# Optimization experiments

Hardware: AMD Instinct MI355X
Metric: run time of the kernel (lower is better)

Reference implementation:

```python
import jax, jax.numpy as jnp
import numpy as np

B, Q, K, A, H, C, O = 32, 512, 512, 256, 8, 32, 256  # batch, queries, keys, channels, heads, head_dim, out_dim


def setup_inputs() -> dict:
    key = jax.random.key(0)
    ks = jax.random.split(key, 12)
    s = 0.02
    return {
        "q_data": jax.random.normal(ks[0], (B, Q, A), jnp.float32),
        "m_data": jax.random.normal(ks[1], (B, K, A), jnp.float32),
        "bias": jax.random.normal(ks[2], (B, 1, 1, K), jnp.float32),
        "nonbatched_bias": jax.random.normal(ks[3], (H, Q, K), jnp.float32),
        "batched_bias": jax.random.normal(ks[4], (B, H, Q, K), jnp.float32),
        "query_w": jax.random.normal(ks[5], (A, H, C), jnp.float32) * s,
        "key_w": jax.random.normal(ks[6], (A, H, C), jnp.float32) * s,
        "value_w": jax.random.normal(ks[7], (A, H, C), jnp.float32) * s,
        "gating_w": jax.random.normal(ks[8], (A, H, C), jnp.float32) * s,
        "gating_b": jnp.ones((H, C), jnp.float32),
        "output_w": jax.random.normal(ks[9], (H, C, O), jnp.float32) * s,
        "output_b": jnp.zeros((O,), jnp.float32),
    }


def reference(q_data, m_data, bias, nonbatched_bias, batched_bias,
              query_w, key_w, value_w, gating_w, gating_b, output_w, output_b):
    key_scale = query_w.shape[-1] ** -0.5
    q = jnp.einsum('bqa,ahc->bqhc', q_data, query_w) * key_scale
    k = jnp.einsum('bka,ahc->bkhc', m_data, key_w)
    v = jnp.einsum('bka,ahc->bkhc', m_data, value_w)
    logits = jnp.einsum('bqhc,bkhc->bhqk', q, k) + bias
    logits = logits + nonbatched_bias[None] + batched_bias
    weights = jax.nn.softmax(logits, axis=-1)
    weighted_avg = jnp.einsum('bhqk,bkhc->bqhc', weights, v)
    gate = jax.nn.sigmoid(jnp.einsum('bqc,chv->bqhv', q_data, gating_w) + gating_b)
    weighted_avg = weighted_avg * gate
    return jnp.einsum('bqhc,hco->bqo', weighted_avg, output_w) + output_b
```

## Files before the change

### kernel.cpp

```cpp
#include <hip/hip_runtime.h>
#include <cstdint>
#include <cstddef>


typedef __attribute__((ext_vector_type(8))) short short8;
typedef __attribute__((ext_vector_type(4))) float f32x4;
typedef __attribute__((ext_vector_type(4))) unsigned int u32x4;
typedef __attribute__((ext_vector_type(2))) unsigned int u32x2;

#define DEVFN static __device__ __forceinline__
#define L2E 1.4426950408889634f

DEVFN unsigned short f2b(float f) {
  unsigned int u = __builtin_bit_cast(unsigned int, f);
  u += 0x7fffu + ((u >> 16) & 1u);
  return (unsigned short)(u >> 16);
}
DEVFN float b2f(unsigned int bits16) {
  return __builtin_bit_cast(float, bits16 << 16);
}
DEVFN unsigned int pack2(float a, float b) {
  return (unsigned int)f2b(a) | ((unsigned int)f2b(b) << 16);
}
DEVFN f32x4 mfma16(short8 a, short8 b, f32x4 c) {
  return __builtin_amdgcn_mfma_f32_16x16x32_bf16(a, b, c, 0, 0, 0);
}

__global__ __launch_bounds__(256) void wtrans_kernel(
    const float* __restrict__ qw, const float* __restrict__ kw,
    const float* __restrict__ vw, const float* __restrict__ gw,
    const float* __restrict__ ow,
    unsigned short* __restrict__ wtq, unsigned short* __restrict__ wtk,
    unsigned short* __restrict__ wtv, unsigned short* __restrict__ wtg,
    unsigned short* __restrict__ wt3)
{
  const int matid = blockIdx.x >> 4;
  const int tile  = blockIdx.x & 15;
  const float* src = (matid == 0) ? qw : (matid == 1) ? kw : (matid == 2) ? vw
                   : (matid == 3) ? gw : ow;
  unsigned short* dst = (matid == 0) ? wtq : (matid == 1) ? wtk : (matid == 2) ? wtv
                      : (matid == 3) ? wtg : wt3;
  const int tr = (tile >> 2) * 64, tc = (tile & 3) * 64;
  __shared__ unsigned short T[64 * 72];
  const int t = threadIdx.x;
  {
    const int row = t >> 2, cb = (t & 3) * 16;
#pragma unroll
    for (int ii = 0; ii < 4; ++ii) {
      f32x4 v = *(const f32x4*)&src[(size_t)(tr + row) * 256 + tc + cb + ii * 4];
      u32x2 p; p.x = pack2(v.x, v.y); p.y = pack2(v.z, v.w);
      *(u32x2*)&T[row * 72 + cb + ii * 4] = p;
    }
  }
  __syncthreads();
  {
    const int c0 = t >> 2, rb = (t & 3) * 16;
    unsigned short vals[16];
#pragma unroll
    for (int m = 0; m < 16; ++m) vals[m] = T[(rb + m) * 72 + c0];
    u32x4 s0, s1;
    s0.x = (unsigned)vals[0]  | ((unsigned)vals[1]  << 16);
    s0.y = (unsigned)vals[2]  | ((unsigned)vals[3]  << 16);
    s0.z = (unsigned)vals[4]  | ((unsigned)vals[5]  << 16);
    s0.w = (unsigned)vals[6]  | ((unsigned)vals[7]  << 16);
    s1.x = (unsigned)vals[8]  | ((unsigned)vals[9]  << 16);
    s1.y = (unsigned)vals[10] | ((unsigned)vals[11] << 16);
    s1.z = (unsigned)vals[12] | ((unsigned)vals[13] << 16);
    s1.w = (unsigned)vals[14] | ((unsigned)vals[15] << 16);
    unsigned short* dp = &dst[(size_t)(tc + c0) * 256 + tr + rb];
    *(u32x4*)dp = s0;
    *(u32x4*)(dp + 8) = s1;
  }
}

__global__ __launch_bounds__(512, 4) void proj_kernel(
    const float* __restrict__ q_data, const float* __restrict__ m_data,
    const unsigned short* __restrict__ wtq, const unsigned short* __restrict__ wtk,
    const unsigned short* __restrict__ wtv, const unsigned short* __restrict__ wtg,
    const float* __restrict__ gating_b,
    unsigned short* __restrict__ qp, unsigned short* __restrict__ kp,
    unsigned short* __restrict__ vp, unsigned short* __restrict__ gate)
{
  const int bid = blockIdx.x;
  const bool mside = bid >= 256;
  const int r0 = (mside ? bid - 256 : bid) * 64;
  const float* inp = mside ? m_data : q_data;
  __shared__ unsigned short Alds[64 * 264];
  __shared__ unsigned short Wlds[2][256 * 40];
  const int t = threadIdx.x;
  const int lane = t & 63, wave = t >> 6;
  const int l15 = lane & 15, g = lane >> 4;
  const int stripe = wave & 3, nhalf = wave >> 2;

  {
    const int row = t >> 3, cb = (t & 7) * 32;
    const float* ip = &inp[(size_t)(r0 + row) * 256 + cb];
#pragma unroll
    for (int i = 0; i < 4; ++i) {
      f32x4 a0 = *(const f32x4*)&ip[i * 8];
      f32x4 a1 = *(const f32x4*)&ip[i * 8 + 4];
      u32x4 pk;
      pk.x = pack2(a0.x, a0.y); pk.y = pack2(a0.z, a0.w);
      pk.z = pack2(a1.x, a1.y); pk.w = pack2(a1.z, a1.w);
      *(u32x4*)&Alds[row * 264 + cb + i * 8] = pk;
    }
  }

  const unsigned short* wt0 = mside ? wtk : wtq;
  const unsigned short* wt1 = mside ? wtv : wtg;
  const int wrow = t & 255, whalf = t >> 8;

  {
    const u32x4* wsrc = (const u32x4*)&wt0[(size_t)wrow * 256 + whalf * 16];
    u32x4 a = wsrc[0], b = wsrc[1];
    *(u32x4*)&Wlds[0][wrow * 40 + whalf * 16 + 0] = a;
    *(u32x4*)&Wlds[0][wrow * 40 + whalf * 16 + 8] = b;
  }

  f32x4 acc[8];
#pragma unroll
  for (int j = 0; j < 8; ++j) acc[j] = f32x4{0.f, 0.f, 0.f, 0.f};

  const int arow = (stripe * 16 + l15) * 264 + 8 * g;
  const int grow = r0 + stripe * 16 + l15;
  const int ob = grow >> 9, oq = grow & 511;

#pragma unroll
  for (int s = 0; s < 16; ++s) {
    const int p = s & 1;
    __syncthreads();
    u32x4 nw0, nw1;
    if (s < 15) {
      const unsigned short* wt = (s + 1 < 8) ? wt0 : wt1;
      const u32x4* wsrc =
          (const u32x4*)&wt[(size_t)wrow * 256 + ((s + 1) & 7) * 32 + whalf * 16];
      nw0 = wsrc[0]; nw1 = wsrc[1];
    }
    const int ks = s & 7;
    short8 bf = __builtin_bit_cast(short8, *(const u32x4*)&Alds[arow + ks * 32]);
#pragma unroll
    for (int j = 0; j < 8; ++j) {
      short8 wf = __builtin_bit_cast(short8,
          *(const u32x4*)&Wlds[p][((nhalf * 8 + j) * 16 + l15) * 40 + 8 * g]);
      acc[j] = mfma16(wf, bf, acc[j]);
    }
    if (s < 15) {
      *(u32x4*)&Wlds[p ^ 1][wrow * 40 + whalf * 16 + 0] = nw0;
      *(u32x4*)&Wlds[p ^ 1][wrow * 40 + whalf * 16 + 8] = nw1;
    }
    if (s == 7 || s == 15) {
      const int oi = s >> 3;
#pragma unroll
      for (int j = 0; j < 8; ++j) {
        const int n0 = (nhalf * 8 + j) * 16 + 4 * g;
        const int h = n0 >> 5, c0 = n0 & 31;
        const size_t idx = ((size_t)(ob * 8 + h) * 512 + oq) * 32 + c0;
        f32x4 v = acc[j];
        if (!mside) {
          if (oi == 0) {
            u32x2 st;
            st.x = pack2(v.x * 0.17677669529663687f, v.y * 0.17677669529663687f);
            st.y = pack2(v.z * 0.17677669529663687f, v.w * 0.17677669529663687f);
            *(u32x2*)&qp[idx] = st;
          } else {
            f32x4 gb = *(const f32x4*)&gating_b[n0];
            f32x4 gv;
            gv.x = 1.0f / (1.0f + exp2f(-(v.x + gb.x) * L2E));
            gv.y = 1.0f / (1.0f + exp2f(-(v.y + gb.y) * L2E));
            gv.z = 1.0f / (1.0f + exp2f(-(v.z + gb.z) * L2E));
            gv.w = 1.0f / (1.0f + exp2f(-(v.w + gb.w) * L2E));
            u32x2 st;
            st.x = pack2(gv.x, gv.y); st.y = pack2(gv.z, gv.w);
            *(u32x2*)&gate[idx] = st;
          }
        } else {
          u32x2 st;
          st.x = pack2(v.x, v.y); st.y = pack2(v.z, v.w);
          if (oi == 0) *(u32x2*)&kp[idx] = st;
          else         *(u32x2*)&vp[idx] = st;
        }
        acc[j] = f32x4{0.f, 0.f, 0.f, 0.f};
      }
    }
  }
}

__global__ __launch_bounds__(512, 4) void attn_kernel(
    const unsigned short* __restrict__ qp, const unsigned short* __restrict__ kp,
    const unsigned short* __restrict__ vp,
    const float* __restrict__ bias, const float* __restrict__ nbias,
    const float* __restrict__ bbias,
    unsigned short* __restrict__ wa)
{
  const int bid = blockIdx.x;
  const int h = bid & 7;
  const int qh = (bid >> 3) & 1;
  const int b = bid >> 4;
  const int bh = b * 8 + h;
  const int t = threadIdx.x;
  const int lane = t & 63, wave = t >> 6;
  const int l15 = lane & 15, g = lane >> 4;

  __shared__ unsigned short Klds[512 * 40];
  __shared__ unsigned short Vt[32 * 520];

  {
    const int row = t;
    const u32x4* ks = (const u32x4*)&kp[((size_t)bh * 512 + row) * 32];
    u32x4 k0 = ks[0], k1 = ks[1], k2 = ks[2], k3 = ks[3];
    *(u32x4*)&Klds[row * 40 + 0]  = k0;
    *(u32x4*)&Klds[row * 40 + 8]  = k1;
    *(u32x4*)&Klds[row * 40 + 16] = k2;
    *(u32x4*)&Klds[row * 40 + 24] = k3;
    const u32x4* vs = (const u32x4*)&vp[((size_t)bh * 512 + row) * 32];
#pragma unroll
    for (int cc = 0; cc < 4; ++cc) {
      u32x4 vv = vs[cc];
      unsigned int dw0 = vv.x, dw1 = vv.y, dw2 = vv.z, dw3 = vv.w;
      const int c = cc * 8;
      Vt[(c + 0) * 520 + row] = (unsigned short)(dw0 & 0xffff);
      Vt[(c + 1) * 520 + row] = (unsigned short)(dw0 >> 16);
      Vt[(c + 2) * 520 + row] = (unsigned short)(dw1 & 0xffff);
      Vt[(c + 3) * 520 + row] = (unsigned short)(dw1 >> 16);
      Vt[(c + 4) * 520 + row] = (unsigned short)(dw2 & 0xffff);
      Vt[(c + 5) * 520 + row] = (unsigned short)(dw2 >> 16);
      Vt[(c + 6) * 520 + row] = (unsigned short)(dw3 & 0xffff);
      Vt[(c + 7) * 520 + row] = (unsigned short)(dw3 >> 16);
    }
  }

  const int qbase = qh * 256 + wave * 32;
  short8 qf[2];
#pragma unroll
  for (int qt = 0; qt < 2; ++qt)
    qf[qt] = __builtin_bit_cast(short8,
        *(const u32x4*)&qp[((size_t)bh * 512 + qbase + qt * 16 + l15) * 32 + 8 * g]);

  const float* bbp = bbias + (size_t)bh * 512 * 512;
  const float* nbp = nbias + (size_t)h * 512 * 512;
  const float* bkp = bias + (size_t)b * 512;

  f32x4 acc[2][2];
#pragma unroll
  for (int ct = 0; ct < 2; ++ct)
#pragma unroll
    for (int qt = 0; qt < 2; ++qt) acc[ct][qt] = f32x4{0.f, 0.f, 0.f, 0.f};
  float l_r[2] = {0.f, 0.f};

  __syncthreads();

  const int pib = ((g & 1) << 4) | ((g >> 1) << 3);
  const bool godd = (g & 1) != 0;

  for (int kt = 0; kt < 16; ++kt) {
    const int k0 = kt * 32;
    short8 kf0 = __builtin_bit_cast(short8, *(const u32x4*)&Klds[(k0 + l15) * 40 + 8 * g]);
    short8 kf1 = __builtin_bit_cast(short8, *(const u32x4*)&Klds[(k0 + 16 + l15) * 40 + 8 * g]);
    short8 vf0 = __builtin_bit_cast(short8, *(const u32x4*)&Vt[l15 * 520 + k0 + pib]);
    short8 vf1 = __builtin_bit_cast(short8, *(const u32x4*)&Vt[(16 + l15) * 520 + k0 + pib]);
    f32x4 bk0 = *(const f32x4*)&bkp[k0 + 4 * g];
    f32x4 bk1 = *(const f32x4*)&bkp[k0 + 16 + 4 * g];
#pragma unroll
    for (int qt = 0; qt < 2; ++qt) {
      const int q = qbase + qt * 16 + l15;
      const float* bq = &bbp[(size_t)q * 512 + k0 + 4 * g];
      const float* nq = &nbp[(size_t)q * 512 + k0 + 4 * g];
      f32x4 bb0 = *(const f32x4*)bq;
      f32x4 bb1 = *(const f32x4*)(bq + 16);
      f32x4 nb0 = *(const f32x4*)nq;
      f32x4 nb1 = *(const f32x4*)(nq + 16);
      f32x4 c0 = (bb0 + nb0) + bk0;
      f32x4 c1 = (bb1 + nb1) + bk1;
      f32x4 s0 = mfma16(kf0, qf[qt], c0);
      f32x4 s1 = mfma16(kf1, qf[qt], c1);
      f32x4 p0, p1;
      p0.x = exp2f(s0.x * L2E); p0.y = exp2f(s0.y * L2E);
      p0.z = exp2f(s0.z * L2E); p0.w = exp2f(s0.w * L2E);
      p1.x = exp2f(s1.x * L2E); p1.y = exp2f(s1.y * L2E);
      p1.z = exp2f(s1.z * L2E); p1.w = exp2f(s1.w * L2E);
      float sum8 = (p0.x + p0.y) + (p0.z + p0.w) + (p1.x + p1.y) + (p1.z + p1.w);
      sum8 += __shfl_xor(sum8, 16, 64);
      sum8 += __shfl_xor(sum8, 32, 64);
      l_r[qt] += sum8;
      unsigned int d0 = pack2(p0.x, p0.y), d1 = pack2(p0.z, p0.w);
      unsigned int e0 = pack2(p1.x, p1.y), e1 = pack2(p1.z, p1.w);
      unsigned int pd0 = __shfl_xor(d0, 16, 64), pd1 = __shfl_xor(d1, 16, 64);
      unsigned int pe0 = __shfl_xor(e0, 16, 64), pe1 = __shfl_xor(e1, 16, 64);
      u32x4 pfu;
      pfu.x = godd ? pe0 : d0;
      pfu.y = godd ? pe1 : d1;
      pfu.z = godd ? e0 : pd0;
      pfu.w = godd ? e1 : pd1;
      short8 pf = __builtin_bit_cast(short8, pfu);
      acc[0][qt] = mfma16(vf0, pf, acc[0][qt]);
      acc[1][qt] = mfma16(vf1, pf, acc[1][qt]);
    }
  }

  unsigned short* wab = wa + (size_t)bh * 512 * 32;
#pragma unroll
  for (int qt = 0; qt < 2; ++qt) {
    const float rl = 1.0f / l_r[qt];
    const int q = qbase + qt * 16 + l15;
#pragma unroll
    for (int ct = 0; ct < 2; ++ct) {
      f32x4 v = acc[ct][qt];
      u32x2 st;
      st.x = pack2(v.x * rl, v.y * rl);
      st.y = pack2(v.z * rl, v.w * rl);
      *(u32x2*)&wab[q * 32 + ct * 16 + 4 * g] = st;
    }
  }
}

__global__ __launch_bounds__(256, 2) void outp_kernel(
    const unsigned short* __restrict__ wa, const unsigned short* __restrict__ gate,
    const unsigned short* __restrict__ wt3, const float* __restrict__ out_b,
    float* __restrict__ out)
{
  const int r0 = blockIdx.x * 32;
  const int t = threadIdx.x;
  const int lane = t & 63, wave = t >> 6;
  const int l15 = lane & 15, g = lane >> 4;
  const int stripe = wave & 1, half = wave >> 1;
  __shared__ unsigned short Wlds[2][256 * 40];

  const int grow = r0 + stripe * 16 + l15;
  const int b = grow >> 9, q = grow & 511;

  {
    const u32x4* wsrc = (const u32x4*)&wt3[(size_t)t * 256];
    u32x4 a = wsrc[0], bb = wsrc[1], c = wsrc[2], d = wsrc[3];
    *(u32x4*)&Wlds[0][t * 40 + 0]  = a;
    *(u32x4*)&Wlds[0][t * 40 + 8]  = bb;
    *(u32x4*)&Wlds[0][t * 40 + 16] = c;
    *(u32x4*)&Wlds[0][t * 40 + 24] = d;
  }
  size_t aidx = ((size_t)(b * 8 + 0) * 512 + q) * 32 + 8 * g;
  u32x4 cwv = *(const u32x4*)&wa[aidx];
  u32x4 cgv = *(const u32x4*)&gate[aidx];

  f32x4 acc[8];
#pragma unroll
  for (int j = 0; j < 8; ++j) acc[j] = f32x4{0.f, 0.f, 0.f, 0.f};

#pragma unroll
  for (int s = 0; s < 8; ++s) {
    const int p = s & 1;
    __syncthreads();
    u32x4 nw0, nw1, nw2, nw3, nwv, ngv;
    if (s < 7) {
      const u32x4* wsrc = (const u32x4*)&wt3[(size_t)t * 256 + (s + 1) * 32];
      nw0 = wsrc[0]; nw1 = wsrc[1]; nw2 = wsrc[2]; nw3 = wsrc[3];
      const size_t na = ((size_t)(b * 8 + s + 1) * 512 + q) * 32 + 8 * g;
      nwv = *(const u32x4*)&wa[na];
      ngv = *(const u32x4*)&gate[na];
    }
    float f0 = b2f(cwv.x & 0xffff) * b2f(cgv.x & 0xffff);
    float f1 = b2f(cwv.x >> 16)    * b2f(cgv.x >> 16);
    float f2 = b2f(cwv.y & 0xffff) * b2f(cgv.y & 0xffff);
    float f3 = b2f(cwv.y >> 16)    * b2f(cgv.y >> 16);
    float f4 = b2f(cwv.z & 0xffff) * b2f(cgv.z & 0xffff);
    float f5 = b2f(cwv.z >> 16)    * b2f(cgv.z >> 16);
    float f6 = b2f(cwv.w & 0xffff) * b2f(cgv.w & 0xffff);
    float f7 = b2f(cwv.w >> 16)    * b2f(cgv.w >> 16);
    u32x4 au;
    au.x = pack2(f0, f1); au.y = pack2(f2, f3);
    au.z = pack2(f4, f5); au.w = pack2(f6, f7);
    short8 af = __builtin_bit_cast(short8, au);
#pragma unroll
    for (int j = 0; j < 8; ++j) {
      short8 wf = __builtin_bit_cast(short8,
          *(const u32x4*)&Wlds[p][((half * 8 + j) * 16 + l15) * 40 + 8 * g]);
      acc[j] = mfma16(wf, af, acc[j]);
    }
    if (s < 7) {
      *(u32x4*)&Wlds[p ^ 1][t * 40 + 0]  = nw0;
      *(u32x4*)&Wlds[p ^ 1][t * 40 + 8]  = nw1;
      *(u32x4*)&Wlds[p ^ 1][t * 40 + 16] = nw2;
      *(u32x4*)&Wlds[p ^ 1][t * 40 + 24] = nw3;
      cwv = nwv; cgv = ngv;
    }
  }
#pragma unroll
  for (int j = 0; j < 8; ++j) {
    const int o0 = (half * 8 + j) * 16 + 4 * g;
    f32x4 ob4 = *(const f32x4*)&out_b[o0];
    f32x4 v = acc[j] + ob4;
    *(f32x4*)&out[(size_t)grow * 256 + o0] = v;
  }
}

extern "C" void kernel_launch(void* const* d_in, const int* in_sizes, int n_in,
                              void* d_out, int out_size, void* d_ws, size_t ws_size,
                              hipStream_t stream)
{
  const float* q_data   = (const float*)d_in[0];
  const float* m_data   = (const float*)d_in[1];
  const float* bias     = (const float*)d_in[2];
  const float* nbb      = (const float*)d_in[3];
  const float* bbb      = (const float*)d_in[4];
  const float* query_w  = (const float*)d_in[5];
  const float* key_w    = (const float*)d_in[6];
  const float* value_w  = (const float*)d_in[7];
  const float* gating_w = (const float*)d_in[8];
  const float* gating_b = (const float*)d_in[9];
  const float* output_w = (const float*)d_in[10];
  const float* output_b = (const float*)d_in[11];
  float* out = (float*)d_out;

  const size_t QP_B   = (size_t)32 * 8 * 512 * 32 * 2;
  const size_t GATE_B = (size_t)32 * 8 * 512 * 32 * 2;
  const size_t WT_B   = (size_t)256 * 256 * 2;

  char* ws = (char*)d_ws;
  unsigned short* qp  = (unsigned short*)(ws);
  unsigned short* kp  = (unsigned short*)(ws + QP_B);
  unsigned short* vp  = (unsigned short*)(ws + 2 * QP_B);
  unsigned short* wab = (unsigned short*)(ws + 3 * QP_B);
  unsigned short* gat = (unsigned short*)(ws + 4 * QP_B);
  unsigned short* wtq = (unsigned short*)(ws + 4 * QP_B + GATE_B);
  unsigned short* wtk = (unsigned short*)(ws + 4 * QP_B + GATE_B + WT_B);
  unsigned short* wtv = (unsigned short*)(ws + 4 * QP_B + GATE_B + 2 * WT_B);
  unsigned short* wtg = (unsigned short*)(ws + 4 * QP_B + GATE_B + 3 * WT_B);
  unsigned short* wt3 = (unsigned short*)(ws + 4 * QP_B + GATE_B + 4 * WT_B);
  const size_t need = 4 * QP_B + GATE_B + 5 * WT_B;
  if (ws_size < need) return;

  hipLaunchKernelGGL(wtrans_kernel, dim3(80), dim3(256), 0, stream,
                     query_w, key_w, value_w, gating_w, output_w,
                     wtq, wtk, wtv, wtg, wt3);
  hipLaunchKernelGGL(proj_kernel, dim3(512), dim3(512), 0, stream,
                     q_data, m_data, wtq, wtk, wtv, wtg, gating_b,
                     qp, kp, vp, gat);
  hipLaunchKernelGGL(attn_kernel, dim3(512), dim3(512), 0, stream,
                     qp, kp, vp, bias, nbb, bbb, wab);
  hipLaunchKernelGGL(outp_kernel, dim3(512), dim3(256), 0, stream,
                     wab, gat, wt3, output_b, out);
}
```

Before: 135.7 us.

## Fold log2e into logits, prefetch bias tiles, defer row-sum shuffles, use hardware bf16 pack

Scales q by log2(e) in the projection and pre-scales the biases so the attention loop can call exp2 directly, without a per-element multiply. The key bias is staged in LDS. Batched and nonbatched bias loads for the first query tile are software-prefetched one iteration ahead. The cross-lane reduction of the softmax denominator moves out of the key loop and runs once at the end, and bf16 packing now uses the v_cvt_pk_bf16_f32 instruction instead of integer rounding code. These changes cut ALU and shuffle work per iteration and hide global-load latency, at the cost of slightly higher register pressure.

```diff
diff --git a/kernel.cpp b/kernel.cpp
--- a/kernel.cpp
+++ b/kernel.cpp
@@ -11,16 +11,13 @@
 #define DEVFN static __device__ __forceinline__
 #define L2E 1.4426950408889634f
 
-DEVFN unsigned short f2b(float f) {
-  unsigned int u = __builtin_bit_cast(unsigned int, f);
-  u += 0x7fffu + ((u >> 16) & 1u);
-  return (unsigned short)(u >> 16);
-}
 DEVFN float b2f(unsigned int bits16) {
   return __builtin_bit_cast(float, bits16 << 16);
 }
 DEVFN unsigned int pack2(float a, float b) {
-  return (unsigned int)f2b(a) | ((unsigned int)f2b(b) << 16);
+  unsigned int r;
+  asm("v_cvt_pk_bf16_f32 %0, %1, %2" : "=v"(r) : "v"(a), "v"(b));
+  return r;
 }
 DEVFN f32x4 mfma16(short8 a, short8 b, f32x4 c) {
   return __builtin_amdgcn_mfma_f32_16x16x32_bf16(a, b, c, 0, 0, 0);
@@ -150,6 +147,7 @@
     }
     if (s == 7 || s == 15) {
       const int oi = s >> 3;
+      const float QS = 0.17677669529663687f * 1.4426950408889634f;
 #pragma unroll
       for (int j = 0; j < 8; ++j) {
         const int n0 = (nhalf * 8 + j) * 16 + 4 * g;
@@ -159,8 +157,8 @@
         if (!mside) {
           if (oi == 0) {
             u32x2 st;
-            st.x = pack2(v.x * 0.17677669529663687f, v.y * 0.17677669529663687f);
-            st.y = pack2(v.z * 0.17677669529663687f, v.w * 0.17677669529663687f);
+            st.x = pack2(v.x * QS, v.y * QS);
+            st.y = pack2(v.z * QS, v.w * QS);
             *(u32x2*)&qp[idx] = st;
           } else {
             f32x4 gb = *(const f32x4*)&gating_b[n0];
@@ -203,6 +201,7 @@
 
   __shared__ unsigned short Klds[512 * 40];
   __shared__ unsigned short Vt[32 * 520];
+  __shared__ float Bk[512];
 
   {
     const int row = t;
@@ -227,6 +226,11 @@
       Vt[(c + 6) * 520 + row] = (unsigned short)(dw3 & 0xffff);
       Vt[(c + 7) * 520 + row] = (unsigned short)(dw3 >> 16);
     }
+    if (t < 128) {
+      f32x4 bv = *(const f32x4*)&bias[(size_t)b * 512 + t * 4];
+      bv.x *= L2E; bv.y *= L2E; bv.z *= L2E; bv.w *= L2E;
+      *(f32x4*)&Bk[t * 4] = bv;
+    }
   }
 
   const int qbase = qh * 256 + wave * 32;
@@ -236,16 +240,22 @@
     qf[qt] = __builtin_bit_cast(short8,
         *(const u32x4*)&qp[((size_t)bh * 512 + qbase + qt * 16 + l15) * 32 + 8 * g]);
 
-  const float* bbp = bbias + (size_t)bh * 512 * 512;
-  const float* nbp = nbias + (size_t)h * 512 * 512;
-  const float* bkp = bias + (size_t)b * 512;
+  const float* b0p = bbias + (size_t)bh * 512 * 512 + (size_t)(qbase + l15) * 512 + 4 * g;
+  const float* b1p = b0p + 16 * 512;
+  const float* n0p = nbias + (size_t)h * 512 * 512 + (size_t)(qbase + l15) * 512 + 4 * g;
+  const float* n1p = n0p + 16 * 512;
 
   f32x4 acc[2][2];
 #pragma unroll
   for (int ct = 0; ct < 2; ++ct)
 #pragma unroll
     for (int qt = 0; qt < 2; ++qt) acc[ct][qt] = f32x4{0.f, 0.f, 0.f, 0.f};
-  float l_r[2] = {0.f, 0.f};
+  float l_part[2] = {0.f, 0.f};
+
+  f32x4 Abb0 = *(const f32x4*)(b0p);
+  f32x4 Abb1 = *(const f32x4*)(b0p + 16);
+  f32x4 Anb0 = *(const f32x4*)(n0p);
+  f32x4 Anb1 = *(const f32x4*)(n0p + 16);
 
   __syncthreads();
 
@@ -258,30 +268,35 @@
     short8 kf1 = __builtin_bit_cast(short8, *(const u32x4*)&Klds[(k0 + 16 + l15) * 40 + 8 * g]);
     short8 vf0 = __builtin_bit_cast(short8, *(const u32x4*)&Vt[l15 * 520 + k0 + pib]);
     short8 vf1 = __builtin_bit_cast(short8, *(const u32x4*)&Vt[(16 + l15) * 520 + k0 + pib]);
-    f32x4 bk0 = *(const f32x4*)&bkp[k0 + 4 * g];
-    f32x4 bk1 = *(const f32x4*)&bkp[k0 + 16 + 4 * g];
+    f32x4 bks0 = *(const f32x4*)&Bk[k0 + 4 * g];
+    f32x4 bks1 = *(const f32x4*)&Bk[k0 + 16 + 4 * g];
+    f32x4 Bbb0 = *(const f32x4*)(b1p + k0);
+    f32x4 Bbb1 = *(const f32x4*)(b1p + k0 + 16);
+    f32x4 Bnb0 = *(const f32x4*)(n1p + k0);
+    f32x4 Bnb1 = *(const f32x4*)(n1p + k0 + 16);
+
 #pragma unroll
     for (int qt = 0; qt < 2; ++qt) {
-      const int q = qbase + qt * 16 + l15;
-      const float* bq = &bbp[(size_t)q * 512 + k0 + 4 * g];
-      const float* nq = &nbp[(size_t)q * 512 + k0 + 4 * g];
-      f32x4 bb0 = *(const f32x4*)bq;
-      f32x4 bb1 = *(const f32x4*)(bq + 16);
-      f32x4 nb0 = *(const f32x4*)nq;
-      f32x4 nb1 = *(const f32x4*)(nq + 16);
-      f32x4 c0 = (bb0 + nb0) + bk0;
-      f32x4 c1 = (bb1 + nb1) + bk1;
+      f32x4 bb0, bb1, nb0, nb1;
+      if (qt == 0) { bb0 = Abb0; bb1 = Abb1; nb0 = Anb0; nb1 = Anb1; }
+      else         { bb0 = Bbb0; bb1 = Bbb1; nb0 = Bnb0; nb1 = Bnb1; }
+      f32x4 c0 = bb0 * L2E + (nb0 * L2E + bks0);
+      f32x4 c1 = bb1 * L2E + (nb1 * L2E + bks1);
       f32x4 s0 = mfma16(kf0, qf[qt], c0);
       f32x4 s1 = mfma16(kf1, qf[qt], c1);
+      if (qt == 0 && kt < 15) {
+        Abb0 = *(const f32x4*)(b0p + k0 + 32);
+        Abb1 = *(const f32x4*)(b0p + k0 + 48);
+        Anb0 = *(const f32x4*)(n0p + k0 + 32);
+        Anb1 = *(const f32x4*)(n0p + k0 + 48);
+      }
       f32x4 p0, p1;
-      p0.x = exp2f(s0.x * L2E); p0.y = exp2f(s0.y * L2E);
-      p0.z = exp2f(s0.z * L2E); p0.w = exp2f(s0.w * L2E);
-      p1.x = exp2f(s1.x * L2E); p1.y = exp2f(s1.y * L2E);
-      p1.z = exp2f(s1.z * L2E); p1.w = exp2f(s1.w * L2E);
-      float sum8 = (p0.x + p0.y) + (p0.z + p0.w) + (p1.x + p1.y) + (p1.z + p1.w);
-      sum8 += __shfl_xor(sum8, 16, 64);
-      sum8 += __shfl_xor(sum8, 32, 64);
-      l_r[qt] += sum8;
+      p0.x = exp2f(s0.x); p0.y = exp2f(s0.y);
+      p0.z = exp2f(s0.z); p0.w = exp2f(s0.w);
+      p1.x = exp2f(s1.x); p1.y = exp2f(s1.y);
+      p1.z = exp2f(s1.z); p1.w = exp2f(s1.w);
+      l_part[qt] += ((p0.x + p0.y) + (p0.z + p0.w)) +
+                    ((p1.x + p1.y) + (p1.z + p1.w));
       unsigned int d0 = pack2(p0.x, p0.y), d1 = pack2(p0.z, p0.w);
       unsigned int e0 = pack2(p1.x, p1.y), e1 = pack2(p1.z, p1.w);
       unsigned int pd0 = __shfl_xor(d0, 16, 64), pd1 = __shfl_xor(d1, 16, 64);
@@ -300,7 +315,10 @@
   unsigned short* wab = wa + (size_t)bh * 512 * 32;
 #pragma unroll
   for (int qt = 0; qt < 2; ++qt) {
-    const float rl = 1.0f / l_r[qt];
+    float l = l_part[qt];
+    l += __shfl_xor(l, 16, 64);
+    l += __shfl_xor(l, 32, 64);
+    const float rl = 1.0f / l;
     const int q = qbase + qt * 16 + l15;
 #pragma unroll
     for (int ct = 0; ct < 2; ++ct) {
```

New measurement: 133.0 us. 2.0% less time.
